# Kernel optimization log

Hardware: AMD Instinct MI355X
Metric: run time of the kernel (lower is better)

## Reference

```python
import jax, jax.numpy as jnp
import numpy as np

N = 100_000   # nodes
E = 600_000   # edges
D = 128       # embed_dim
G = 1000      # graphs (batch ids)
L = 3         # num_layers


def setup_inputs() -> dict:
    key = jax.random.key(0)
    ks = jax.random.split(key, 12)
    s = 1.0 / np.sqrt(D)
    return {
        "x": jax.random.normal(ks[0], (N, D), jnp.float32),
        "edge_index": jax.random.randint(ks[1], (2, E), 0, N),
        "batch": jnp.sort(jax.random.randint(ks[2], (N,), 0, G)),
        "mask": jax.random.randint(ks[3], (N,), 0, 2),
        # stacked GCNConv weights/biases (in=hidden=out=D)
        "gcn_w": jax.random.normal(ks[4], (L, D, D), jnp.float32) * s,
        "gcn_b": jnp.zeros((L, D), jnp.float32),
        # MLP head: Linear(D,D) -> ReLU -> Linear(D,1)
        "lin1_w": jax.random.normal(ks[5], (D, D), jnp.float32) * s,
        "lin1_b": jnp.zeros((D,), jnp.float32),
        "lin2_w": jax.random.normal(ks[6], (D,), jnp.float32) * s,
        "lin2_b": jnp.zeros((), jnp.float32),
    }


def gcn_forward(x, src, dst, gcn_w, gcn_b):
    # symmetric gcn_norm with self-loops: deg[i] = 1 + in-degree(i)
    deg = jax.ops.segment_sum(jnp.ones((E,), x.dtype), dst, num_segments=N) + 1.0
    dinv = jax.lax.rsqrt(deg)
    enorm = dinv[src] * dinv[dst]          # [E] edge normalization
    self_norm = (dinv * dinv)[:, None]     # [N,1] self-loop normalization
    h = x
    for l in range(L):
        h = h @ gcn_w[l]                   # [N,D]
        h = (jax.ops.segment_sum(h[src] * enorm[:, None], dst, num_segments=N)
             + h * self_norm)
        h = h + gcn_b[l]
        if l < L - 1:
            h = jax.nn.relu(h)  # (dropout inactive at inference)
    return h


def reference(x, edge_index, batch, mask, gcn_w, gcn_b, lin1_w, lin1_b, lin2_w, lin2_b):
    src, dst = edge_index[0], edge_index[1]
    h = gcn_forward(x, src, dst, gcn_w, gcn_b)
    # MLP head -> per-node score [N]
    s = jax.nn.relu(h @ lin1_w + lin1_b) @ lin2_w + lin2_b
    s = jnp.where(mask == 0, jnp.float32(-1e9), s)
    # per-graph (segment) softmax — fused replacement for the unique/batch loop
    m = jax.ops.segment_max(s, batch, num_segments=G)
    e = jnp.exp(s - m[batch])
    z = jax.ops.segment_sum(e, batch, num_segments=G)
    return e / z[batch]
```

## Files before the change

### kernel.cpp

```cpp
#include <hip/hip_runtime.h>
#include <hip/hip_bf16.h>

typedef unsigned int u32;
typedef unsigned short u16;
typedef __attribute__((ext_vector_type(8))) short bf16x8;
typedef __attribute__((ext_vector_type(4))) float f32x4;

__device__ __forceinline__ float u16tof(u16 u){ return __uint_as_float(((u32)u) << 16); }
__device__ __forceinline__ float lo16(u32 v){ return __uint_as_float(v << 16); }
__device__ __forceinline__ float hi16(u32 v){ return __uint_as_float(v & 0xffff0000u); }
__device__ __forceinline__ u16 ftobf(float f){
  u32 b = __float_as_uint(f);
  return (u16)((b + 0x7FFFu + ((b >> 16) & 1u)) >> 16);
}
__device__ __forceinline__ u32 pack2(float a, float b){
  return (u32)ftobf(a) | ((u32)ftobf(b) << 16);
}
__device__ __forceinline__ float ldf(const void* p, int i, int isbf){
  return isbf ? u16tof(((const u16*)p)[i]) : ((const float*)p)[i];
}

__device__ __forceinline__ void acc8(float* a, uint4 v, float mk){
  a[0] = fmaf(lo16(v.x), mk, a[0]);
  a[1] = fmaf(hi16(v.x), mk, a[1]);
  a[2] = fmaf(lo16(v.y), mk, a[2]);
  a[3] = fmaf(hi16(v.y), mk, a[3]);
  a[4] = fmaf(lo16(v.z), mk, a[4]);
  a[5] = fmaf(hi16(v.z), mk, a[5]);
  a[6] = fmaf(lo16(v.w), mk, a[6]);
  a[7] = fmaf(hi16(v.w), mk, a[7]);
}

__device__ __forceinline__ void gather2(const u16* __restrict__ Tin, const int* __restrict__ eid,
                                        int jA, int eA, int jB, int eB, int l16,
                                        float* a, float* b){
  while (jA < eA || jB < eB){
    int sA[4], sB[4];
    #pragma unroll
    for (int k = 0; k < 4; ++k){
      const int iA = jA + k; sA[k] = eid[iA < eA ? iA : 0];
      const int iB = jB + k; sB[k] = eid[iB < eB ? iB : 0];
    }
    uint4 vA[4], vB[4];
    #pragma unroll
    for (int k = 0; k < 4; ++k) vA[k] = ((const uint4*)(Tin + (size_t)sA[k] * 128))[l16];
    #pragma unroll
    for (int k = 0; k < 4; ++k) vB[k] = ((const uint4*)(Tin + (size_t)sB[k] * 128))[l16];
    #pragma unroll
    for (int k = 0; k < 4; ++k){
      acc8(a, vA[k], (jA + k < eA) ? 1.f : 0.f);
      acc8(b, vB[k], (jB + k < eB) ? 1.f : 0.f);
    }
    jA += 4; jB += 4;
  }
}

__global__ __launch_bounds__(256) void k_prep(const void* __restrict__ gw, const void* __restrict__ l1w,
                                              const void* __restrict__ x, u16* __restrict__ Wf,
                                              u16* __restrict__ Hb, int L, int n8, int cvtB, int goffB,
                                              const int* __restrict__ batch, int* __restrict__ goff,
                                              int N, int G,
                                              const int* __restrict__ dst, int* __restrict__ hist,
                                              int nE, int chunk, int* __restrict__ flag){
  __shared__ int sh[256];
  const int b = blockIdx.x;
  const int t = threadIdx.x;
  const int histStart = L + 1 + cvtB + goffB;

  if (b >= histStart){
    sh[t] = 0; __syncthreads();
    const int blk = b - histStart;
    const int e0 = blk * chunk, e1 = min(e0 + chunk, nE);
    for (int e = e0 + t; e < e1; e += 256) atomicAdd(&sh[dst[e] >> 9], 1);
    __syncthreads();
    hist[blk * 256 + t] = sh[t];
    return;
  }
  if (b >= L + 1 + cvtB){
    const int i = (b - (L + 1 + cvtB)) * 256 + t;
    if (i >= N) return;
    const int bt = batch[i];
    const int prev = (i == 0) ? -1 : batch[i - 1];
    for (int g = prev + 1; g <= bt; ++g) goff[g] = i;
    if (i == N - 1){ for (int g = bt + 1; g <= G; ++g) goff[g] = N; }
    return;
  }
  if (t == 0) sh[0] = 0;
  __syncthreads();
  if (b <= L){
    int local = 0;
    for (int i = t; i < 4096; i += 256){
      u32 e = (((const u32*)gw)[i] >> 7) & 0xFFu;
      if (e >= 100u && e < 127u) local++;
    }
    atomicAdd(&sh[0], local);
    __syncthreads();
    const int isbf = (sh[0] > 2048) ? 1 : 0;
    if (b == 0 && t == 0) *flag = isbf;

    const void* src = (b < L) ? gw : l1w;
    const int sbase = (b < L) ? b * 16384 : 0;
    u16* dstp = Wf + (size_t)b * 16384;
    for (int g = t; g < 2048; g += 256){
      const int tt = g >> 8, ks = (g >> 6) & 3, lane = g & 63;
      const int n = tt * 16 + (lane & 15);
      const int k0 = ks * 32 + ((lane >> 4) << 3);
      u16* d = dstp + (size_t)g * 8;
      #pragma unroll
      for (int j = 0; j < 8; ++j){
        d[j] = ftobf(ldf(src, sbase + (k0 + j) * 128 + n, isbf));
      }
    }
  } else {
    u32 e = (((const u32*)gw)[t] >> 7) & 0xFFu;
    atomicAdd(&sh[0], (e >= 100u && e < 127u) ? 1 : 0);
    __syncthreads();
    if (sh[0] > 128) return;
    const int i = (b - (L + 1)) * 256 + t;
    if (i >= n8) return;
    const float4 a = ((const float4*)x)[i * 2];
    const float4 c = ((const float4*)x)[i * 2 + 1];
    u16* o = Hb + (size_t)i * 8;
    o[0] = ftobf(a.x); o[1] = ftobf(a.y); o[2] = ftobf(a.z); o[3] = ftobf(a.w);
    o[4] = ftobf(c.x); o[5] = ftobf(c.y); o[6] = ftobf(c.z); o[7] = ftobf(c.w);
  }
}

__global__ __launch_bounds__(256) void k_hscan(int* __restrict__ hist, int* __restrict__ bb, int nE){
  const int t = threadIdx.x;
  int run = 0;
  for (int j = 0; j < 256; j += 8){
    int v[8];
    #pragma unroll
    for (int k = 0; k < 8; ++k) v[k] = hist[(j + k) * 256 + t];
    #pragma unroll
    for (int k = 0; k < 8; ++k){
      hist[(j + k) * 256 + t] = run;
      run += v[k];
    }
  }
  __shared__ int sm[256];
  sm[t] = run; __syncthreads();
  for (int off = 1; off < 256; off <<= 1){
    int a = (t >= off) ? sm[t - off] : 0;
    __syncthreads();
    sm[t] += a;
    __syncthreads();
  }
  bb[t] = sm[t] - run;
  if (t == 255) bb[256] = nE;
}

__global__ __launch_bounds__(256) void k_scatter(const int* __restrict__ src, const int* __restrict__ dst,
                                                 const int* __restrict__ hist, const int* __restrict__ bb,
                                                 int2* __restrict__ tmpe, int nE, int chunk){
  __shared__ int base[256];
  const int blk = blockIdx.x, t = threadIdx.x;
  base[t] = bb[t] + hist[blk * 256 + t];
  __syncthreads();
  const int e0 = blk * chunk, e1 = min(e0 + chunk, nE);
  for (int e = e0 + t; e < e1; e += 256){
    const int d = dst[e];
    const int pos = atomicAdd(&base[d >> 9], 1);
    tmpe[pos] = make_int2(src[e], d);
  }
}

__global__ __launch_bounds__(256) void k_local(const int2* __restrict__ tmpe, const int* __restrict__ bb,
                                               int* __restrict__ boff, int* __restrict__ eid,
                                               float* __restrict__ dinv, int N, int nE, int nbkt){
  __shared__ int hcnt[512];
  __shared__ int hoff[512];
  const int b = blockIdx.x, t = threadIdx.x;
  const int n0 = b << 9;
  const int n1 = min(n0 + 512, N);
  const int nn = n1 - n0;
  const int e0 = bb[b], e1 = bb[b + 1];
  hcnt[t] = 0; hcnt[t + 256] = 0;
  __syncthreads();
  for (int e = e0 + t; e < e1; e += 256) atomicAdd(&hcnt[tmpe[e].y - n0], 1);
  __syncthreads();
  const int v0 = hcnt[t], v1 = hcnt[t + 256];
  hoff[t] = v0; hoff[t + 256] = v1;
  __syncthreads();
  for (int off = 1; off < 512; off <<= 1){
    int a0 = (t >= off) ? hoff[t - off] : 0;
    int a1 = (t + 256 >= off) ? hoff[t + 256 - off] : 0;
    __syncthreads();
    hoff[t] += a0; hoff[t + 256] += a1;
    __syncthreads();
  }
  const int ex0 = hoff[t] - v0 + e0;
  const int ex1 = hoff[t + 256] - v1 + e0;
  if (t < nn){       boff[n0 + t] = ex0;        dinv[n0 + t] = rsqrtf((float)v0 + 1.0f); }
  if (t + 256 < nn){ boff[n0 + t + 256] = ex1;  dinv[n0 + t + 256] = rsqrtf((float)v1 + 1.0f); }
  if (b == nbkt - 1 && t == 0) boff[N] = nE;
  __syncthreads();
  hoff[t] = ex0; hoff[t + 256] = ex1;
  __syncthreads();
  for (int e = e0 + t; e < e1; e += 256){
    const int2 pr = tmpe[e];
    const int pos = atomicAdd(&hoff[pr.y - n0], 1);
    eid[pos] = pr.x;
  }
}

__global__ __launch_bounds__(256) void k_mm(const void* __restrict__ X, const u16* __restrict__ Hb,
                                            const u16* __restrict__ Wf, const float* __restrict__ dinv,
                                            u16* __restrict__ T, int n, const int* __restrict__ fl){
  __shared__ u16 smw[16384];
  const int isbf = *fl;
  const u16* A = isbf ? (const u16*)X : Hb;
  {
    const uint4* s = (const uint4*)Wf;
    uint4* d = (uint4*)smw;
    for (int i = threadIdx.x; i < 2048; i += 256) d[i] = s[i];
  }
  __syncthreads();

  const int wave = threadIdx.x >> 6, lane = threadIdx.x & 63;
  const int m0 = blockIdx.x * 64 + wave * 16;
  int arow = m0 + (lane & 15); if (arow > n - 1) arow = n - 1;
  const u16* aptr = A + (size_t)arow * 128 + ((lane >> 4) << 3);

  f32x4 acc[8];
  #pragma unroll
  for (int t = 0; t < 8; ++t) acc[t] = (f32x4){0.f, 0.f, 0.f, 0.f};

  #pragma unroll
  for (int ks = 0; ks < 4; ++ks){
    const bf16x8 a = *(const bf16x8*)(aptr + ks * 32);
    #pragma unroll
    for (int t = 0; t < 8; ++t){
      const bf16x8 b = *(const bf16x8*)(smw + (size_t)(((t * 4 + ks) * 64 + lane) * 8));
      acc[t] = __builtin_amdgcn_mfma_f32_16x16x32_bf16(a, b, acc[t], 0, 0, 0);
    }
  }
  __syncthreads();

  const int quad = lane >> 4, col0 = lane & 15;
  float dv[4];
  #pragma unroll
  for (int r = 0; r < 4; ++r){
    const int row = m0 + quad * 4 + r;
    dv[r] = (row < n) ? dinv[row] : 0.f;
  }
  u16* my = smw + wave * 2112;
  #pragma unroll
  for (int t = 0; t < 8; ++t){
    #pragma unroll
    for (int r = 0; r < 4; ++r){
      my[(quad * 4 + r) * 132 + t * 16 + col0] = ftobf(acc[t][r] * dv[r]);
    }
  }
  #pragma unroll
  for (int i = 0; i < 4; ++i){
    const int row = i * 4 + (lane >> 4);
    const int grow = m0 + row;
    const int c8 = (lane & 15) * 8;
    if (grow < n){
      const u16* s = &my[row * 132 + c8];
      uint2 lo = *(const uint2*)(s);
      uint2 hi = *(const uint2*)(s + 4);
      *(uint4*)&T[(size_t)grow * 128 + c8] = make_uint4(lo.x, lo.y, hi.x, hi.y);
    }
  }
}

__global__ __launch_bounds__(256) void k_gmm(const u16* __restrict__ Tin, const int* __restrict__ boff,
                                             const int* __restrict__ eid, const float* __restrict__ dinv,
                                             const void* __restrict__ bias, int layer,
                                             const u16* __restrict__ Wf, u16* __restrict__ Tout,
                                             int n, const int* __restrict__ fl){
  __shared__ u16 sma[32 * 132];
  const int isbf = *fl;
  const int tid = threadIdx.x;
  const int wave = tid >> 6, lane = tid & 63;
  const int sub = lane >> 4, l16 = lane & 15;
  const int m0 = blockIdx.x * 32;

  const int nA = m0 + wave * 8 + sub;
  const int nB = nA + 4;
  float a[8], b[8];
  #pragma unroll
  for (int k = 0; k < 8; ++k){ a[k] = 0.f; b[k] = 0.f; }
  int jA = 0, eA = 0, jB = 0, eB = 0;
  if (nA < n){ jA = boff[nA]; eA = boff[nA + 1]; }
  if (nB < n){ jB = boff[nB]; eB = boff[nB + 1]; }
  if (nA < n){
    const uint4 sv = ((const uint4*)(Tin + (size_t)nA * 128))[l16];
    acc8(a, sv, 1.f);
  }
  if (nB < n){
    const uint4 sv = ((const uint4*)(Tin + (size_t)nB * 128))[l16];
    acc8(b, sv, 1.f);
  }
  gather2(Tin, eid, jA, eA, jB, eB, l16, a, b);

  const int bb = layer * 128 + l16 * 8;
  if (nA < n){
    const float di = dinv[nA];
    #pragma unroll
    for (int k = 0; k < 8; ++k) a[k] = fmaxf(fmaf(a[k], di, ldf(bias, bb + k, isbf)), 0.f);
  }
  if (nB < n){
    const float di = dinv[nB];
    #pragma unroll
    for (int k = 0; k < 8; ++k) b[k] = fmaxf(fmaf(b[k], di, ldf(bias, bb + k, isbf)), 0.f);
  }
  {
    uint4 oA, oB;
    oA.x = pack2(a[0], a[1]); oA.y = pack2(a[2], a[3]); oA.z = pack2(a[4], a[5]); oA.w = pack2(a[6], a[7]);
    oB.x = pack2(b[0], b[1]); oB.y = pack2(b[2], b[3]); oB.z = pack2(b[4], b[5]); oB.w = pack2(b[6], b[7]);
    *(uint4*)&sma[(wave * 8 + sub) * 132 + l16 * 8] = oA;
    *(uint4*)&sma[(wave * 8 + sub + 4) * 132 + l16 * 8] = oB;
  }
  __syncthreads();

  const int r0 = (wave & 1) * 16;
  const int cg = wave >> 1;
  f32x4 acc[4];
  #pragma unroll
  for (int tt = 0; tt < 4; ++tt) acc[tt] = (f32x4){0.f, 0.f, 0.f, 0.f};
  #pragma unroll
  for (int ks = 0; ks < 4; ++ks){
    const bf16x8 av = *(const bf16x8*)(sma + (r0 + l16) * 132 + sub * 8 + ks * 32);
    #pragma unroll
    for (int tt = 0; tt < 4; ++tt){
      const int t = cg * 4 + tt;
      const bf16x8 bv = *(const bf16x8*)(Wf + (size_t)(((t * 4 + ks) * 64 + lane) * 8));
      acc[tt] = __builtin_amdgcn_mfma_f32_16x16x32_bf16(av, bv, acc[tt], 0, 0, 0);
    }
  }
  __syncthreads();

  float dv[4];
  #pragma unroll
  for (int r = 0; r < 4; ++r){
    const int row = m0 + r0 + sub * 4 + r;
    dv[r] = (row < n) ? dinv[row] : 0.f;
  }
  #pragma unroll
  for (int tt = 0; tt < 4; ++tt){
    #pragma unroll
    for (int r = 0; r < 4; ++r){
      sma[(r0 + sub * 4 + r) * 132 + (cg * 4 + tt) * 16 + l16] = ftobf(acc[tt][r] * dv[r]);
    }
  }
  __syncthreads();

  #pragma unroll
  for (int i = 0; i < 2; ++i){
    const int idx = tid + i * 256;
    const int row = idx >> 4;
    const int c8 = (idx & 15) * 8;
    if (m0 + row < n){
      const u16* s = &sma[row * 132 + c8];
      uint2 lo = *(const uint2*)(s);
      uint2 hi = *(const uint2*)(s + 4);
      *(uint4*)&Tout[(size_t)(m0 + row) * 128 + c8] = make_uint4(lo.x, lo.y, hi.x, hi.y);
    }
  }
}

__global__ __launch_bounds__(256) void k_ghead(const u16* __restrict__ Tin, const int* __restrict__ boff,
                                               const int* __restrict__ eid, const float* __restrict__ dinv,
                                               const void* __restrict__ bias, int layer,
                                               const u16* __restrict__ Wf, const void* __restrict__ b1,
                                               const void* __restrict__ w2, const void* __restrict__ b2,
                                               const int* __restrict__ mask, float* __restrict__ s,
                                               int n, const int* __restrict__ fl){
  __shared__ u16 sma[32 * 132];
  __shared__ float sred[4][16];
  const int isbf = *fl;
  const int tid = threadIdx.x;
  const int wave = tid >> 6, lane = tid & 63;
  const int sub = lane >> 4, l16 = lane & 15;
  const int m0 = blockIdx.x * 32;

  const int nA = m0 + wave * 8 + sub;
  const int nB = nA + 4;
  float a[8], b[8];
  #pragma unroll
  for (int k = 0; k < 8; ++k){ a[k] = 0.f; b[k] = 0.f; }
  int jA = 0, eA = 0, jB = 0, eB = 0;
  if (nA < n){ jA = boff[nA]; eA = boff[nA + 1]; }
  if (nB < n){ jB = boff[nB]; eB = boff[nB + 1]; }
  if (nA < n){
    const uint4 sv = ((const uint4*)(Tin + (size_t)nA * 128))[l16];
    acc8(a, sv, 1.f);
  }
  if (nB < n){
    const uint4 sv = ((const uint4*)(Tin + (size_t)nB * 128))[l16];
    acc8(b, sv, 1.f);
  }
  gather2(Tin, eid, jA, eA, jB, eB, l16, a, b);

  const int bb = layer * 128 + l16 * 8;
  if (nA < n){
    const float di = dinv[nA];
    #pragma unroll
    for (int k = 0; k < 8; ++k) a[k] = fmaf(a[k], di, ldf(bias, bb + k, isbf));
  }
  if (nB < n){
    const float di = dinv[nB];
    #pragma unroll
    for (int k = 0; k < 8; ++k) b[k] = fmaf(b[k], di, ldf(bias, bb + k, isbf));
  }
  {
    uint4 oA, oB;
    oA.x = pack2(a[0], a[1]); oA.y = pack2(a[2], a[3]); oA.z = pack2(a[4], a[5]); oA.w = pack2(a[6], a[7]);
    oB.x = pack2(b[0], b[1]); oB.y = pack2(b[2], b[3]); oB.z = pack2(b[4], b[5]); oB.w = pack2(b[6], b[7]);
    *(uint4*)&sma[(wave * 8 + sub) * 132 + l16 * 8] = oA;
    *(uint4*)&sma[(wave * 8 + sub + 4) * 132 + l16 * 8] = oB;
  }
  __syncthreads();

  const int r0 = (wave & 1) * 16;
  const int cg = wave >> 1;
  f32x4 acc[4];
  #pragma unroll
  for (int tt = 0; tt < 4; ++tt) acc[tt] = (f32x4){0.f, 0.f, 0.f, 0.f};
  #pragma unroll
  for (int ks = 0; ks < 4; ++ks){
    const bf16x8 av = *(const bf16x8*)(sma + (r0 + l16) * 132 + sub * 8 + ks * 32);
    #pragma unroll
    for (int tt = 0; tt < 4; ++tt){
      const int t = cg * 4 + tt;
      const bf16x8 bv = *(const bf16x8*)(Wf + (size_t)(((t * 4 + ks) * 64 + lane) * 8));
      acc[tt] = __builtin_amdgcn_mfma_f32_16x16x32_bf16(av, bv, acc[tt], 0, 0, 0);
    }
  }

  float p0 = 0.f, p1 = 0.f, p2 = 0.f, p3 = 0.f;
  #pragma unroll
  for (int tt = 0; tt < 4; ++tt){
    const int col = (cg * 4 + tt) * 16 + l16;
    const float bv = ldf(b1, col, isbf);
    const float wv = ldf(w2, col, isbf);
    p0 = fmaf(fmaxf(acc[tt][0] + bv, 0.f), wv, p0);
    p1 = fmaf(fmaxf(acc[tt][1] + bv, 0.f), wv, p1);
    p2 = fmaf(fmaxf(acc[tt][2] + bv, 0.f), wv, p2);
    p3 = fmaf(fmaxf(acc[tt][3] + bv, 0.f), wv, p3);
  }
  #pragma unroll
  for (int k = 1; k < 16; k <<= 1){
    p0 += __shfl_xor(p0, k);
    p1 += __shfl_xor(p1, k);
    p2 += __shfl_xor(p2, k);
    p3 += __shfl_xor(p3, k);
  }
  if (l16 == 0){
    sred[wave][sub * 4 + 0] = p0;
    sred[wave][sub * 4 + 1] = p1;
    sred[wave][sub * 4 + 2] = p2;
    sred[wave][sub * 4 + 3] = p3;
  }
  __syncthreads();
  if (tid < 32){
    const int row = m0 + tid;
    if (row < n){
      const int rg = tid >> 4, idx = tid & 15;
      float sc = sred[rg][idx] + sred[rg + 2][idx] + ldf(b2, 0, isbf);
      if (mask[row] == 0) sc = -1e9f;
      s[row] = sc;
    }
  }
}

__global__ __launch_bounds__(256) void k_gsm(const float* __restrict__ s, const int* __restrict__ goff,
                                             void* __restrict__ out, int G, const int* __restrict__ fl){
  const int g = blockIdx.x * 4 + (threadIdx.x >> 6);
  if (g >= G) return;
  const int lane = threadIdx.x & 63;
  const int i0 = goff[g], i1 = goff[g + 1];
  if (i0 >= i1) return;
  float m = -3.4e38f;
  for (int j = i0 + lane; j < i1; j += 64) m = fmaxf(m, s[j]);
  #pragma unroll
  for (int k = 32; k; k >>= 1) m = fmaxf(m, __shfl_xor(m, k));
  float zz = 0.f;
  for (int j = i0 + lane; j < i1; j += 64) zz += expf(s[j] - m);
  #pragma unroll
  for (int k = 32; k; k >>= 1) zz += __shfl_xor(zz, k);
  const float rz = 1.f / zz;
  const int isbf = *fl;
  for (int j = i0 + lane; j < i1; j += 64){
    const float v = expf(s[j] - m) * rz;
    if (isbf) ((u16*)out)[j] = ftobf(v);
    else      ((float*)out)[j] = v;
  }
}

extern "C" void kernel_launch(void* const* d_in, const int* in_sizes, int n_in,
                              void* d_out, int out_size, void* d_ws, size_t ws_size,
                              hipStream_t stream){
  const void* x    = d_in[0];
  const int* ei    = (const int*)d_in[1];
  const int* batch = (const int*)d_in[2];
  const int* mask  = (const int*)d_in[3];
  const void* gw   = d_in[4];
  const void* gb   = d_in[5];
  const void* l1w  = d_in[6];
  const void* l1b  = d_in[7];
  const void* l2w  = d_in[8];
  const void* l2b  = d_in[9];

  const int N = in_sizes[2];
  const int E = in_sizes[1] / 2;
  const int D = 128;
  const int L = in_sizes[4] / (D * D);
  const int G = 1000;

  char* p = (char*)d_ws;
  u16*  Hb    = (u16*)p;   p += (size_t)N * D * sizeof(u16);
  u16*  Tb    = (u16*)p;   p += (size_t)N * D * sizeof(u16);
  u16*  Wf    = (u16*)p;   p += (size_t)(L + 1) * D * D * sizeof(u16);
  float* dinv = (float*)p; p += (size_t)N * sizeof(float);
  float* sbuf = (float*)p; p += (size_t)N * sizeof(float);
  int*  boff  = (int*)p;   p += (size_t)(N + 1) * sizeof(int);
  int*  eid   = (int*)p;   p += (size_t)E * sizeof(int);
  int*  goff  = (int*)p;   p += (size_t)(G + 1) * sizeof(int);
  int*  hist  = (int*)p;   p += 256 * 256 * sizeof(int);
  int*  bb    = (int*)p;   p += 260 * sizeof(int);
  int2* tmpe  = (int2*)p;  p += (size_t)E * sizeof(int2);
  int*  flag  = (int*)p;   p += 256;

  const int* srcp = ei;
  const int* dstp = ei + E;

  const int mmg   = (N + 63) / 64;
  const int fg    = (N + 31) / 32;
  const int n8    = N * D / 8;
  const int cvtB  = (n8 + 255) / 256;
  const int goffB = (N + 255) / 256;
  const int chunk = (E + 255) / 256;
  const int nbkt  = (N + 511) / 512;

  k_prep<<<(L + 1) + cvtB + goffB + 256, 256, 0, stream>>>(gw, l1w, x, Wf, Hb, L, n8, cvtB, goffB,
                                                           batch, goff, N, G, dstp, hist, E, chunk, flag);
  k_hscan<<<1, 256, 0, stream>>>(hist, bb, E);
  k_scatter<<<256, 256, 0, stream>>>(srcp, dstp, hist, bb, tmpe, E, chunk);
  k_local<<<nbkt, 256, 0, stream>>>(tmpe, bb, boff, eid, dinv, N, E, nbkt);

  k_mm<<<mmg, 256, 0, stream>>>(x, Hb, Wf, dinv, Tb, N, flag);
  k_gmm<<<fg, 256, 0, stream>>>(Tb, boff, eid, dinv, gb, 0, Wf + (size_t)1 * D * D, Hb, N, flag);
  k_gmm<<<fg, 256, 0, stream>>>(Hb, boff, eid, dinv, gb, 1, Wf + (size_t)2 * D * D, Tb, N, flag);
  k_ghead<<<fg, 256, 0, stream>>>(Tb, boff, eid, dinv, gb, 2, Wf + (size_t)L * D * D,
                                  l1b, l2w, l2b, mask, sbuf, N, flag);
  k_gsm<<<(G + 3) / 4, 256, 0, stream>>>(sbuf, goff, d_out, G, flag);
}
```

Measured before the change: 344.5 us.

## Stage edge ids in LDS and software-pipeline neighbor row gathers

Each block first copies its contiguous CSR edge-id range into shared memory, so the gather reads source ids from LDS rather than global memory. The gather loop is restructured to double-buffer eight 16-byte row loads, issuing the next batch before accumulating the current one. Both changes aim to hide gather latency and raise memory-level parallelism. In exchange they add 12KB of LDS per block, which can lower occupancy, plus an extra block-wide barrier, and twice as many live uint4 registers.

```diff
diff --git a/kernel.cpp b/kernel.cpp
--- a/kernel.cpp
+++ b/kernel.cpp
@@ -31,28 +31,45 @@
   a[7] = fmaf(hi16(v.w), mk, a[7]);
 }
 
-__device__ __forceinline__ void gather2(const u16* __restrict__ Tin, const int* __restrict__ eid,
-                                        int jA, int eA, int jB, int eB, int l16,
-                                        float* a, float* b){
-  while (jA < eA || jB < eB){
-    int sA[4], sB[4];
+__device__ __forceinline__ void gather_pipe(const u16* __restrict__ Tin,
+                                            const int* __restrict__ eid,
+                                            const int* __restrict__ seid, int inlds, int e0,
+                                            int jA0, int eAe, int jB0, int eBe,
+                                            int l16, float* a, float* b){
+  const int dA = eAe - jA0, dB = eBe - jB0;
+  const int dmax = dA > dB ? dA : dB;
+  if (dmax <= 0) return;
+  const int T = (dmax + 3) >> 2;
+  uint4 P[8], Q[8];
+
+  auto issue = [&](uint4* X, int o){
+    int id[8];
     #pragma unroll
     for (int k = 0; k < 4; ++k){
-      const int iA = jA + k; sA[k] = eid[iA < eA ? iA : 0];
-      const int iB = jB + k; sB[k] = eid[iB < eB ? iB : 0];
-    }
-    uint4 vA[4], vB[4];
-    #pragma unroll
-    for (int k = 0; k < 4; ++k) vA[k] = ((const uint4*)(Tin + (size_t)sA[k] * 128))[l16];
-    #pragma unroll
-    for (int k = 0; k < 4; ++k) vB[k] = ((const uint4*)(Tin + (size_t)sB[k] * 128))[l16];
+      int pA = jA0 + o + k; pA = (pA < eAe) ? pA : e0;
+      int pB = jB0 + o + k; pB = (pB < eBe) ? pB : e0;
+      id[k]     = inlds ? seid[pA - e0] : eid[pA];
+      id[k + 4] = inlds ? seid[pB - e0] : eid[pB];
+    }
+    #pragma unroll
+    for (int k = 0; k < 8; ++k) X[k] = ((const uint4*)(Tin + (size_t)id[k] * 128))[l16];
+  };
+  auto accum = [&](uint4* X, int o){
     #pragma unroll
     for (int k = 0; k < 4; ++k){
-      acc8(a, vA[k], (jA + k < eA) ? 1.f : 0.f);
-      acc8(b, vB[k], (jB + k < eB) ? 1.f : 0.f);
-    }
-    jA += 4; jB += 4;
-  }
+      acc8(a, X[k],     (jA0 + o + k < eAe) ? 1.f : 0.f);
+      acc8(b, X[k + 4], (jB0 + o + k < eBe) ? 1.f : 0.f);
+    }
+  };
+
+  issue(P, 0);
+  for (int t = 0; t + 1 < T; t += 2){
+    issue(Q, (t + 1) * 4);
+    accum(P, t * 4);
+    if (t + 2 < T) issue(P, (t + 2) * 4);
+    accum(Q, (t + 1) * 4);
+  }
+  if (T & 1) accum(P, (T - 1) * 4);
 }
 
 __global__ __launch_bounds__(256) void k_prep(const void* __restrict__ gw, const void* __restrict__ l1w,
@@ -273,20 +290,30 @@
                                              const u16* __restrict__ Wf, u16* __restrict__ Tout,
                                              int n, const int* __restrict__ fl){
   __shared__ u16 sma[32 * 132];
+  __shared__ int seid[3072];
   const int isbf = *fl;
   const int tid = threadIdx.x;
   const int wave = tid >> 6, lane = tid & 63;
   const int sub = lane >> 4, l16 = lane & 15;
   const int m0 = blockIdx.x * 32;
+  const int mEnd = min(m0 + 32, n);
+
+  const int e0 = boff[m0];
+  const int e1 = boff[mEnd];
+  const int len = e1 - e0;
+  const int inlds = (len <= 3072) ? 1 : 0;
+  if (inlds){
+    for (int i = tid; i < len; i += 256) seid[i] = eid[e0 + i];
+  }
 
   const int nA = m0 + wave * 8 + sub;
   const int nB = nA + 4;
   float a[8], b[8];
   #pragma unroll
   for (int k = 0; k < 8; ++k){ a[k] = 0.f; b[k] = 0.f; }
-  int jA = 0, eA = 0, jB = 0, eB = 0;
-  if (nA < n){ jA = boff[nA]; eA = boff[nA + 1]; }
-  if (nB < n){ jB = boff[nB]; eB = boff[nB + 1]; }
+  int jA0 = 0, eAe = 0, jB0 = 0, eBe = 0;
+  if (nA < n){ jA0 = boff[nA]; eAe = boff[nA + 1]; }
+  if (nB < n){ jB0 = boff[nB]; eBe = boff[nB + 1]; }
   if (nA < n){
     const uint4 sv = ((const uint4*)(Tin + (size_t)nA * 128))[l16];
     acc8(a, sv, 1.f);
@@ -295,7 +322,8 @@
     const uint4 sv = ((const uint4*)(Tin + (size_t)nB * 128))[l16];
     acc8(b, sv, 1.f);
   }
-  gather2(Tin, eid, jA, eA, jB, eB, l16, a, b);
+  __syncthreads();
+  gather_pipe(Tin, eid, seid, inlds, e0, jA0, eAe, jB0, eBe, l16, a, b);
 
   const int bb = layer * 128 + l16 * 8;
   if (nA < n){
@@ -371,21 +399,31 @@
                                                const int* __restrict__ mask, float* __restrict__ s,
                                                int n, const int* __restrict__ fl){
   __shared__ u16 sma[32 * 132];
+  __shared__ int seid[3072];
   __shared__ float sred[4][16];
   const int isbf = *fl;
   const int tid = threadIdx.x;
   const int wave = tid >> 6, lane = tid & 63;
   const int sub = lane >> 4, l16 = lane & 15;
   const int m0 = blockIdx.x * 32;
+  const int mEnd = min(m0 + 32, n);
+
+  const int e0 = boff[m0];
+  const int e1 = boff[mEnd];
+  const int len = e1 - e0;
+  const int inlds = (len <= 3072) ? 1 : 0;
+  if (inlds){
+    for (int i = tid; i < len; i += 256) seid[i] = eid[e0 + i];
+  }
 
   const int nA = m0 + wave * 8 + sub;
   const int nB = nA + 4;
   float a[8], b[8];
   #pragma unroll
   for (int k = 0; k < 8; ++k){ a[k] = 0.f; b[k] = 0.f; }
-  int jA = 0, eA = 0, jB = 0, eB = 0;
-  if (nA < n){ jA = boff[nA]; eA = boff[nA + 1]; }
-  if (nB < n){ jB = boff[nB]; eB = boff[nB + 1]; }
+  int jA0 = 0, eAe = 0, jB0 = 0, eBe = 0;
+  if (nA < n){ jA0 = boff[nA]; eAe = boff[nA + 1]; }
+  if (nB < n){ jB0 = boff[nB]; eBe = boff[nB + 1]; }
   if (nA < n){
     const uint4 sv = ((const uint4*)(Tin + (size_t)nA * 128))[l16];
     acc8(a, sv, 1.f);
@@ -394,7 +432,8 @@
     const uint4 sv = ((const uint4*)(Tin + (size_t)nB * 128))[l16];
     acc8(b, sv, 1.f);
   }
-  gather2(Tin, eid, jA, eA, jB, eB, l16, a, b);
+  __syncthreads();
+  gather_pipe(Tin, eid, seid, inlds, e0, jA0, eAe, jB0, eBe, l16, a, b);
 
   const int bb = layer * 128 + l16 * 8;
   if (nA < n){
```

Result: slower. 352.5 us (+2.3%).
